# Kernel tuning notes

Hardware: AMD Instinct MI355X
Metric: run time of the kernel (lower is better)

The kernel has to match this reference:

```python
import jax, jax.numpy as jnp
import numpy as np


def setup_inputs() -> dict:
    key = jax.random.key(0)
    ks = jax.random.split(key, 6)
    B, Tq, Tk = 4, 512, 512
    Q, K, C = 1024, 1024, 256
    query = jax.random.normal(ks[0], (B, Tq, Q), dtype=jnp.float32)
    kmat = jax.random.normal(ks[1], (B, Tk, K), dtype=jnp.float32)
    # Linear weights (torch nn.Linear stores [out, in]; we keep [in, out] for einsum)
    Wq = jax.random.normal(ks[2], (Q, C), dtype=jnp.float32) / np.sqrt(Q)
    Wk = jax.random.normal(ks[3], (K, C), dtype=jnp.float32) / np.sqrt(K)
    w_attn = jax.random.normal(ks[4], (C,), dtype=jnp.float32) / np.sqrt(C)
    b_attn = jax.random.normal(ks[5], (), dtype=jnp.float32) * 0.01
    return {"query": query, "key": kmat, "Wq": Wq, "Wk": Wk,
            "w_attn": w_attn, "b_attn": b_attn}


def reference(query, key, Wq, Wk, w_attn, b_attn):
    # Additive (Bahdanau) attention scores.
    # q2ctx: (B, Tq, C); k2ctx: (B, Tk, C)
    q2ctx = jnp.einsum('bqi,ic->bqc', query, Wq)
    k2ctx = jnp.einsum('bki,ic->bkc', key, Wk)
    # broadcast add -> (B, Tq, Tk, C), tanh, project to scalar and squeeze
    ctx = jnp.tanh(q2ctx[:, :, None, :] + k2ctx[:, None, :, :])
    scores = jnp.einsum('bqkc,c->bqk', ctx, w_attn) + b_attn
    return scores  # (B, Tq, Tk)
```

## Files before the change

kernel.cpp:

```cpp
#include <hip/hip_runtime.h>

#define M_ROWS 2048
#define KDIM   1024
#define CDIM   256
#define TQ     512
#define TK     512

#define GBM 64
#define GBN 32
#define GBK 32

#define SCALE2LOG2E 2.8853900817779268f

typedef __attribute__((ext_vector_type(8))) short short8;
typedef __attribute__((ext_vector_type(4))) float floatx4;
typedef __attribute__((ext_vector_type(2))) float f32x2;

__device__ __forceinline__ short f2bf(float f) {
    unsigned x = __builtin_bit_cast(unsigned, f);
    unsigned r = (x + 0x7FFFu + ((x >> 16) & 1u)) >> 16;
    return (short)r;
}

__global__ __launch_bounds__(256) void gemm_mfma_kernel(
    const float* __restrict__ Aq, const float* __restrict__ Ak,
    const float* __restrict__ Wq, const float* __restrict__ Wk,
    const float* __restrict__ w_attn,
    float* __restrict__ Eq, float* __restrict__ Ek)
{
    __shared__ short As[GBM][GBK + 8];
    __shared__ short Ws[GBN][GBK + 8];

    const int z = blockIdx.z;
    const float* A = z ? Ak : Aq;
    const float* W = z ? Wk : Wq;
    float*       E = z ? Ek : Eq;

    const int t    = threadIdx.x;
    const int lane = t & 63;
    const int wave = t >> 6;
    const int m0   = blockIdx.x * GBM;
    const int n0   = blockIdx.y * GBN;

    const int ar = t >> 2;
    const int ac = (t & 3) * 8;
    const int wr = t >> 3;
    const int wc = (t & 7) * 4;

    const int iw = wave & 1;
    const int jw = wave >> 1;
    const int li = lane & 15;
    const int qd = lane >> 4;

    floatx4 acc0 = {0.f, 0.f, 0.f, 0.f};
    floatx4 acc1 = {0.f, 0.f, 0.f, 0.f};

    for (int k0 = 0; k0 < KDIM; k0 += GBK) {
        float4 a0 = *(const float4*)&A[(size_t)(m0 + ar) * KDIM + k0 + ac];
        float4 a1 = *(const float4*)&A[(size_t)(m0 + ar) * KDIM + k0 + ac + 4];
        float4 w0 = *(const float4*)&W[(size_t)(k0 + wr) * CDIM + n0 + wc];
        __syncthreads();
        short8 av = { f2bf(a0.x), f2bf(a0.y), f2bf(a0.z), f2bf(a0.w),
                      f2bf(a1.x), f2bf(a1.y), f2bf(a1.z), f2bf(a1.w) };
        *(short8*)&As[ar][ac] = av;
        Ws[wc + 0][wr] = f2bf(w0.x);
        Ws[wc + 1][wr] = f2bf(w0.y);
        Ws[wc + 2][wr] = f2bf(w0.z);
        Ws[wc + 3][wr] = f2bf(w0.w);
        __syncthreads();
        short8 af  = *(const short8*)&Ws[iw * 16 + li][qd * 8];
        short8 bf0 = *(const short8*)&As[jw * 32 + li][qd * 8];
        short8 bf1 = *(const short8*)&As[jw * 32 + 16 + li][qd * 8];
        acc0 = __builtin_amdgcn_mfma_f32_16x16x32_bf16(af, bf0, acc0, 0, 0, 0);
        acc1 = __builtin_amdgcn_mfma_f32_16x16x32_bf16(af, bf1, acc1, 0, 0, 0);
    }

    #pragma unroll
    for (int r = 0; r < 4; ++r) {
        const int c = n0 + iw * 16 + qd * 4 + r;
        float scale = z ? 1.0f : (-0.5f / w_attn[c]);
        float v0 = __builtin_amdgcn_exp2f(acc0[r] * SCALE2LOG2E) * scale;
        float v1 = __builtin_amdgcn_exp2f(acc1[r] * SCALE2LOG2E) * scale;
        E[(size_t)c * M_ROWS + m0 + jw * 32 + li]      = v0;
        E[(size_t)c * M_ROWS + m0 + jw * 32 + 16 + li] = v1;
    }
}

__global__ __launch_bounds__(256) void bahdanau_kernel(
    const float* __restrict__ Eqs, const float* __restrict__ Ek,
    const float* __restrict__ w_attn, const float* __restrict__ b_attn,
    float* __restrict__ out)
{
    __shared__ float qs[64][36];
    __shared__ float ks[64][36];
    __shared__ float sl[CDIM];
    __shared__ float partial[4];

    const int t  = threadIdx.x;
    const int b  = blockIdx.z;
    const int q0 = blockIdx.x * 32;
    const int k0 = blockIdx.y * 32;
    const int gq = b * TQ + q0;
    const int gk = b * TK + k0;
    const int tq = t & 15;
    const int tk = t >> 4;
    const int lr = t >> 3;
    const int lc = (t & 7) * 4;

    {
        float wv = w_attn[t];
        sl[t] = -0.5f / wv;
        float sum = wv;
        #pragma unroll
        for (int o = 32; o >= 1; o >>= 1) sum += __shfl_down(sum, o);
        if ((t & 63) == 0) partial[t >> 6] = sum;
    }

    f32x2 a0 = {0.f, 0.f};
    f32x2 a1 = {0.f, 0.f};

    for (int c0 = 0; c0 < CDIM; c0 += 64) {
        float4 qv0 = *(const float4*)&Eqs[(size_t)(c0 + lr     ) * M_ROWS + gq + lc];
        float4 qv1 = *(const float4*)&Eqs[(size_t)(c0 + lr + 32) * M_ROWS + gq + lc];
        float4 kv0 = *(const float4*)&Ek [(size_t)(c0 + lr     ) * M_ROWS + gk + lc];
        float4 kv1 = *(const float4*)&Ek [(size_t)(c0 + lr + 32) * M_ROWS + gk + lc];
        __syncthreads();
        *(float4*)&qs[lr     ][lc] = qv0;
        *(float4*)&qs[lr + 32][lc] = qv1;
        *(float4*)&ks[lr     ][lc] = kv0;
        *(float4*)&ks[lr + 32][lc] = kv1;
        __syncthreads();
        #pragma unroll 16
        for (int c = 0; c < 64; ++c) {
            f32x2 qp = *(const f32x2*)&qs[c][2 * tq];
            f32x2 kp = *(const f32x2*)&ks[c][2 * tk];
            float s  = sl[c0 + c];
            f32x2 sv  = {s, s};
            f32x2 kxx = {kp.x, kp.x};
            f32x2 kyy = {kp.y, kp.y};
            f32x2 f0 = __builtin_elementwise_fma(qp, kxx, sv);
            f32x2 f1 = __builtin_elementwise_fma(qp, kyy, sv);
            f32x2 r0 = {__builtin_amdgcn_rcpf(f0.x), __builtin_amdgcn_rcpf(f0.y)};
            f32x2 r1 = {__builtin_amdgcn_rcpf(f1.x), __builtin_amdgcn_rcpf(f1.y)};
            a0 += r0;
            a1 += r1;
        }
    }

    const float bias2 = *b_attn + partial[0] + partial[1] + partial[2] + partial[3];
    float* o = out + ((size_t)b * TQ + q0) * TK + k0;
    *(float2*)&o[(2 * tq    ) * TK + 2 * tk] = make_float2(a0.x + bias2, a1.x + bias2);
    *(float2*)&o[(2 * tq + 1) * TK + 2 * tk] = make_float2(a0.y + bias2, a1.y + bias2);
}

extern "C" void kernel_launch(void* const* d_in, const int* in_sizes, int n_in,
                              void* d_out, int out_size, void* d_ws, size_t ws_size,
                              hipStream_t stream) {
    const float* query  = (const float*)d_in[0];
    const float* key    = (const float*)d_in[1];
    const float* Wq     = (const float*)d_in[2];
    const float* Wk     = (const float*)d_in[3];
    const float* w_attn = (const float*)d_in[4];
    const float* b_attn = (const float*)d_in[5];
    float* out = (float*)d_out;

    float* Eqs = (float*)d_ws;
    float* Ek  = Eqs + (size_t)CDIM * M_ROWS;

    dim3 gemm_grid(M_ROWS / GBM, CDIM / GBN, 2);
    gemm_mfma_kernel<<<gemm_grid, 256, 0, stream>>>(query, key, Wq, Wk, w_attn, Eqs, Ek);

    dim3 main_grid(TQ / 32, TK / 32, 4);
    bahdanau_kernel<<<main_grid, 256, 0, stream>>>(Eqs, Ek, w_attn, b_attn, out);
}
```

Baseline: 124.3 us.

## Pair reciprocals algebraically, enlarge attention tile, and prefetch global loads in both kernels

The main kernel now combines two channel terms as (f1+f2)/(f1*f2), so each pair needs one reciprocal instead of two. This cuts the transcendental throughput that bounds the inner loop. The tile grows to 64x32, giving each thread a 4x2 output block, and next-chunk global loads are register-prefetched. The GEMM also prefetches its next k-slice and uses packed bf16 conversion. The product f1*f2 risks overflow or precision loss when terms are large or near zero.

```diff
diff --git a/kernel.cpp b/kernel.cpp
--- a/kernel.cpp
+++ b/kernel.cpp
@@ -1,4 +1,5 @@
 #include <hip/hip_runtime.h>
+#include <hip/hip_bf16.h>
 
 #define M_ROWS 2048
 #define KDIM   1024
@@ -10,16 +11,20 @@
 #define GBN 32
 #define GBK 32
 
+#define QT 64
+#define KT 32
+
 #define SCALE2LOG2E 2.8853900817779268f
 
 typedef __attribute__((ext_vector_type(8))) short short8;
 typedef __attribute__((ext_vector_type(4))) float floatx4;
 typedef __attribute__((ext_vector_type(2))) float f32x2;
 
-__device__ __forceinline__ short f2bf(float f) {
-    unsigned x = __builtin_bit_cast(unsigned, f);
-    unsigned r = (x + 0x7FFFu + ((x >> 16) & 1u)) >> 16;
-    return (short)r;
+__device__ __forceinline__ short2 cvt2(float x, float y) {
+    __hip_bfloat162 h = __float22bfloat162_rn(make_float2(x, y));
+    short2 r;
+    __builtin_memcpy(&r, &h, sizeof(r));
+    return r;
 }
 
 __global__ __launch_bounds__(256) void gemm_mfma_kernel(
@@ -55,19 +60,27 @@
     floatx4 acc0 = {0.f, 0.f, 0.f, 0.f};
     floatx4 acc1 = {0.f, 0.f, 0.f, 0.f};
 
+    float4 a0 = *(const float4*)&A[(size_t)(m0 + ar) * KDIM + ac];
+    float4 a1 = *(const float4*)&A[(size_t)(m0 + ar) * KDIM + ac + 4];
+    float4 w0 = *(const float4*)&W[(size_t)wr * CDIM + n0 + wc];
+
     for (int k0 = 0; k0 < KDIM; k0 += GBK) {
-        float4 a0 = *(const float4*)&A[(size_t)(m0 + ar) * KDIM + k0 + ac];
-        float4 a1 = *(const float4*)&A[(size_t)(m0 + ar) * KDIM + k0 + ac + 4];
-        float4 w0 = *(const float4*)&W[(size_t)(k0 + wr) * CDIM + n0 + wc];
-        __syncthreads();
-        short8 av = { f2bf(a0.x), f2bf(a0.y), f2bf(a0.z), f2bf(a0.w),
-                      f2bf(a1.x), f2bf(a1.y), f2bf(a1.z), f2bf(a1.w) };
+        __syncthreads();
+        short2 p0 = cvt2(a0.x, a0.y), p1 = cvt2(a0.z, a0.w);
+        short2 p2 = cvt2(a1.x, a1.y), p3 = cvt2(a1.z, a1.w);
+        short8 av = { p0.x, p0.y, p1.x, p1.y, p2.x, p2.y, p3.x, p3.y };
         *(short8*)&As[ar][ac] = av;
-        Ws[wc + 0][wr] = f2bf(w0.x);
-        Ws[wc + 1][wr] = f2bf(w0.y);
-        Ws[wc + 2][wr] = f2bf(w0.z);
-        Ws[wc + 3][wr] = f2bf(w0.w);
-        __syncthreads();
+        short2 u0 = cvt2(w0.x, w0.y), u1 = cvt2(w0.z, w0.w);
+        Ws[wc + 0][wr] = u0.x;
+        Ws[wc + 1][wr] = u0.y;
+        Ws[wc + 2][wr] = u1.x;
+        Ws[wc + 3][wr] = u1.y;
+        __syncthreads();
+        if (k0 + GBK < KDIM) {
+            a0 = *(const float4*)&A[(size_t)(m0 + ar) * KDIM + k0 + GBK + ac];
+            a1 = *(const float4*)&A[(size_t)(m0 + ar) * KDIM + k0 + GBK + ac + 4];
+            w0 = *(const float4*)&W[(size_t)(k0 + GBK + wr) * CDIM + n0 + wc];
+        }
         short8 af  = *(const short8*)&Ws[iw * 16 + li][qd * 8];
         short8 bf0 = *(const short8*)&As[jw * 32 + li][qd * 8];
         short8 bf1 = *(const short8*)&As[jw * 32 + 16 + li][qd * 8];
@@ -91,21 +104,24 @@
     const float* __restrict__ w_attn, const float* __restrict__ b_attn,
     float* __restrict__ out)
 {
-    __shared__ float qs[64][36];
-    __shared__ float ks[64][36];
+    __shared__ float qs[64][QT + 4];
+    __shared__ float ks[64][KT + 4];
     __shared__ float sl[CDIM];
     __shared__ float partial[4];
 
     const int t  = threadIdx.x;
     const int b  = blockIdx.z;
-    const int q0 = blockIdx.x * 32;
-    const int k0 = blockIdx.y * 32;
+    const int q0 = blockIdx.x * QT;
+    const int k0 = blockIdx.y * KT;
     const int gq = b * TQ + q0;
     const int gk = b * TK + k0;
-    const int tq = t & 15;
-    const int tk = t >> 4;
-    const int lr = t >> 3;
-    const int lc = (t & 7) * 4;
+    const int tq = (t >> 4) * 4;
+    const int tk = (t & 15) * 2;
+
+    const int qlr = t >> 4;
+    const int qlc = (t & 15) * 4;
+    const int klr = t >> 3;
+    const int klc = (t & 7) * 4;
 
     {
         float wv = w_attn[t];
@@ -116,41 +132,77 @@
         if ((t & 63) == 0) partial[t >> 6] = sum;
     }
 
-    f32x2 a0 = {0.f, 0.f};
-    f32x2 a1 = {0.f, 0.f};
-
-    for (int c0 = 0; c0 < CDIM; c0 += 64) {
-        float4 qv0 = *(const float4*)&Eqs[(size_t)(c0 + lr     ) * M_ROWS + gq + lc];
-        float4 qv1 = *(const float4*)&Eqs[(size_t)(c0 + lr + 32) * M_ROWS + gq + lc];
-        float4 kv0 = *(const float4*)&Ek [(size_t)(c0 + lr     ) * M_ROWS + gk + lc];
-        float4 kv1 = *(const float4*)&Ek [(size_t)(c0 + lr + 32) * M_ROWS + gk + lc];
-        __syncthreads();
-        *(float4*)&qs[lr     ][lc] = qv0;
-        *(float4*)&qs[lr + 32][lc] = qv1;
-        *(float4*)&ks[lr     ][lc] = kv0;
-        *(float4*)&ks[lr + 32][lc] = kv1;
-        __syncthreads();
-        #pragma unroll 16
-        for (int c = 0; c < 64; ++c) {
-            f32x2 qp = *(const f32x2*)&qs[c][2 * tq];
-            f32x2 kp = *(const f32x2*)&ks[c][2 * tk];
-            float s  = sl[c0 + c];
-            f32x2 sv  = {s, s};
-            f32x2 kxx = {kp.x, kp.x};
-            f32x2 kyy = {kp.y, kp.y};
-            f32x2 f0 = __builtin_elementwise_fma(qp, kxx, sv);
-            f32x2 f1 = __builtin_elementwise_fma(qp, kyy, sv);
-            f32x2 r0 = {__builtin_amdgcn_rcpf(f0.x), __builtin_amdgcn_rcpf(f0.y)};
-            f32x2 r1 = {__builtin_amdgcn_rcpf(f1.x), __builtin_amdgcn_rcpf(f1.y)};
-            a0 += r0;
-            a1 += r1;
+    float4 qv[4], kv[2];
+    #pragma unroll
+    for (int j = 0; j < 4; ++j)
+        qv[j] = *(const float4*)&Eqs[(size_t)(qlr + 16 * j) * M_ROWS + gq + qlc];
+    #pragma unroll
+    for (int j = 0; j < 2; ++j)
+        kv[j] = *(const float4*)&Ek[(size_t)(klr + 32 * j) * M_ROWS + gk + klc];
+
+    f32x2 acc[4] = {{0.f, 0.f}, {0.f, 0.f}, {0.f, 0.f}, {0.f, 0.f}};
+
+    for (int ch = 0; ch < 4; ++ch) {
+        __syncthreads();
+        #pragma unroll
+        for (int j = 0; j < 4; ++j) *(float4*)&qs[qlr + 16 * j][qlc] = qv[j];
+        #pragma unroll
+        for (int j = 0; j < 2; ++j) *(float4*)&ks[klr + 32 * j][klc] = kv[j];
+        __syncthreads();
+        if (ch < 3) {
+            const int c1 = (ch + 1) * 64;
+            #pragma unroll
+            for (int j = 0; j < 4; ++j)
+                qv[j] = *(const float4*)&Eqs[(size_t)(c1 + qlr + 16 * j) * M_ROWS + gq + qlc];
+            #pragma unroll
+            for (int j = 0; j < 2; ++j)
+                kv[j] = *(const float4*)&Ek[(size_t)(c1 + klr + 32 * j) * M_ROWS + gk + klc];
         }
+        const int cb = ch * 64;
+        #pragma unroll 4
+        for (int c = 0; c < 64; c += 2) {
+            float s1v = sl[cb + c], s2v = sl[cb + c + 1];
+            f32x2 s1 = {s1v, s1v}, s2 = {s2v, s2v};
+            float4 q1 = *(const float4*)&qs[c][tq];
+            float4 q2 = *(const float4*)&qs[c + 1][tq];
+            f32x2 k1 = *(const f32x2*)&ks[c][tk];
+            f32x2 k2 = *(const f32x2*)&ks[c + 1][tk];
+            {
+                f32x2 f1 = __builtin_elementwise_fma((f32x2){q1.x, q1.x}, k1, s1);
+                f32x2 f2 = __builtin_elementwise_fma((f32x2){q2.x, q2.x}, k2, s2);
+                f32x2 g = f1 * f2, h = f1 + f2;
+                f32x2 r = {__builtin_amdgcn_rcpf(g.x), __builtin_amdgcn_rcpf(g.y)};
+                acc[0] = __builtin_elementwise_fma(h, r, acc[0]);
+            }
+            {
+                f32x2 f1 = __builtin_elementwise_fma((f32x2){q1.y, q1.y}, k1, s1);
+                f32x2 f2 = __builtin_elementwise_fma((f32x2){q2.y, q2.y}, k2, s2);
+                f32x2 g = f1 * f2, h = f1 + f2;
+                f32x2 r = {__builtin_amdgcn_rcpf(g.x), __builtin_amdgcn_rcpf(g.y)};
+                acc[1] = __builtin_elementwise_fma(h, r, acc[1]);
+            }
+            {
+                f32x2 f1 = __builtin_elementwise_fma((f32x2){q1.z, q1.z}, k1, s1);
+                f32x2 f2 = __builtin_elementwise_fma((f32x2){q2.z, q2.z}, k2, s2);
+                f32x2 g = f1 * f2, h = f1 + f2;
+                f32x2 r = {__builtin_amdgcn_rcpf(g.x), __builtin_amdgcn_rcpf(g.y)};
+                acc[2] = __builtin_elementwise_fma(h, r, acc[2]);
+            }
+            {
+                f32x2 f1 = __builtin_elementwise_fma((f32x2){q1.w, q1.w}, k1, s1);
+                f32x2 f2 = __builtin_elementwise_fma((f32x2){q2.w, q2.w}, k2, s2);
+                f32x2 g = f1 * f2, h = f1 + f2;
+                f32x2 r = {__builtin_amdgcn_rcpf(g.x), __builtin_amdgcn_rcpf(g.y)};
+                acc[3] = __builtin_elementwise_fma(h, r, acc[3]);
+            }
+        }
     }
 
     const float bias2 = *b_attn + partial[0] + partial[1] + partial[2] + partial[3];
-    float* o = out + ((size_t)b * TQ + q0) * TK + k0;
-    *(float2*)&o[(2 * tq    ) * TK + 2 * tk] = make_float2(a0.x + bias2, a1.x + bias2);
-    *(float2*)&o[(2 * tq + 1) * TK + 2 * tk] = make_float2(a0.y + bias2, a1.y + bias2);
+    float* o = out + ((size_t)b * TQ + q0 + tq) * TK + k0 + tk;
+    #pragma unroll
+    for (int i = 0; i < 4; ++i)
+        *(float2*)&o[i * TK] = make_float2(acc[i].x + bias2, acc[i].y + bias2);
 }
 
 extern "C" void kernel_launch(void* const* d_in, const int* in_sizes, int n_in,
@@ -170,6 +222,6 @@
     dim3 gemm_grid(M_ROWS / GBM, CDIM / GBN, 2);
     gemm_mfma_kernel<<<gemm_grid, 256, 0, stream>>>(query, key, Wq, Wk, w_attn, Eqs, Ek);
 
-    dim3 main_grid(TQ / 32, TK / 32, 4);
+    dim3 main_grid(TQ / QT, TK / KT, 4);
     bahdanau_kernel<<<main_grid, 256, 0, stream>>>(Eqs, Ek, w_attn, b_attn, out);
 }
```

Result: no change. 124.5 us (+0.2%).
